# Optimization experiments

Measured on AMD Instinct MI355X. Metric: run time of the kernel, lower is better.

The kernel has to match this reference:

```python
import jax, jax.numpy as jnp
import numpy as np

B, S, D, H = 2, 2048, 1024, 16
DK = D // H


def setup_inputs() -> dict:
    key = jax.random.key(0)
    ks = jax.random.split(key, 6)
    scale = D ** -0.5
    return {
        "x": jax.random.normal(ks[0], (B, S, D), dtype=jnp.float32),
        "Wq": jax.random.normal(ks[1], (D, D), dtype=jnp.float32) * scale,
        "Wk": jax.random.normal(ks[2], (D, D), dtype=jnp.float32) * scale,
        "Wv": jax.random.normal(ks[3], (D, D), dtype=jnp.float32) * scale,
        "Wp": jax.random.normal(ks[4], (D, D), dtype=jnp.float32) * scale,
        "bp": jax.random.normal(ks[5], (D,), dtype=jnp.float32) * 0.01,
    }


def reference(x, Wq, Wk, Wv, Wp, bp):
    b, s, d = x.shape
    # projections (torch Linear: x @ W.T)
    q = (x @ Wq.T).reshape(b, s, H, DK).transpose(0, 2, 1, 3)  # [b,h,s,dk]
    k = (x @ Wk.T).reshape(b, s, H, DK).transpose(0, 2, 1, 3)
    v = (x @ Wv.T).reshape(b, s, H, DK).transpose(0, 2, 1, 3)
    wei = jnp.einsum('bhqd,bhkd->bhqk', q, k) * (DK ** -0.5)  # [b,h,s,s]
    causal = jnp.tril(jnp.ones((s, s), dtype=bool))
    wei = jnp.where(causal, wei, -jnp.inf)
    wei = jax.nn.softmax(wei, axis=-1)
    out = jnp.einsum('bhqk,bhkd->bhqd', wei, v)
    out = out.transpose(0, 2, 1, 3).reshape(b, s, H * DK)
    return out @ Wp.T + bp
```

## Files before the change

kernel.cpp:

```cpp
#include <hip/hip_runtime.h>
#include <hip/hip_bf16.h>

typedef short short8 __attribute__((ext_vector_type(8)));
typedef float floatx4 __attribute__((ext_vector_type(4)));
typedef float floatx16 __attribute__((ext_vector_type(16)));

#define DEV static __device__ __forceinline__

DEV unsigned short f2bf(float x) {
    union { float f; unsigned u; } v; v.f = x;
    unsigned r = v.u + 0x7FFFu + ((v.u >> 16) & 1u);
    return (unsigned short)(r >> 16);
}

DEV unsigned pk2(float lo, float hi) {
    union { __hip_bfloat162 h; unsigned u; } v;
    v.h = __float22bfloat162_rn(make_float2(lo, hi));
    return v.u;
}

DEV float fexp2(float x) {
#if __has_builtin(__builtin_amdgcn_exp2f)
    return __builtin_amdgcn_exp2f(x);
#else
    return exp2f(x);
#endif
}

DEV __attribute__((address_space(3))) unsigned int* lds_as3(void* p) {
    return (__attribute__((address_space(3))) unsigned int*)(unsigned int)(unsigned long long)p;
}
DEV const __attribute__((address_space(1))) unsigned int* gbl_as1(const void* p) {
    return (const __attribute__((address_space(1))) unsigned int*)(unsigned long long)p;
}

__global__ __launch_bounds__(256) void cvt_all(
    const float* __restrict__ x,  const float* __restrict__ wq,
    const float* __restrict__ wk, const float* __restrict__ wv,
    const float* __restrict__ wp,
    unsigned short* __restrict__ xb, unsigned short* __restrict__ wqkv,
    unsigned short* __restrict__ wpb)
{
    long c = (long)blockIdx.x * 256 + threadIdx.x;
    const float* src; unsigned short* dst; long off;
    if      (c <  524288) { src = x;  dst = xb;             off = c;          }
    else if (c <  655360) { src = wq; dst = wqkv;           off = c - 524288; }
    else if (c <  786432) { src = wk; dst = wqkv + 1048576; off = c - 655360; }
    else if (c <  917504) { src = wv; dst = wqkv + 2097152; off = c - 786432; }
    else                  { src = wp; dst = wpb;            off = c - 917504; }
    float4 a = ((const float4*)src)[off * 2];
    float4 b = ((const float4*)src)[off * 2 + 1];
    ushort4 r0, r1;
    r0.x = f2bf(a.x); r0.y = f2bf(a.y); r0.z = f2bf(a.z); r0.w = f2bf(a.w);
    r1.x = f2bf(b.x); r1.y = f2bf(b.y); r1.z = f2bf(b.z); r1.w = f2bf(b.w);
    ((ushort4*)dst)[off * 2]     = r0;
    ((ushort4*)dst)[off * 2 + 1] = r1;
}

template <int EPI>
__global__ __launch_bounds__(256) void gemm_bt(
    const unsigned short* __restrict__ A, const unsigned short* __restrict__ Bw,
    int M, int N, int K,
    unsigned short* __restrict__ Qd, unsigned short* __restrict__ Kd,
    unsigned short* __restrict__ Vtd,
    float* __restrict__ Cout, const float* __restrict__ bias)
{
    __shared__ unsigned short As[128 * 32];
    __shared__ unsigned short Bs[128 * 32];
    const int t    = threadIdx.x;
    const int lane = t & 63;
    const int wv   = t >> 6;
    const int wr   = (wv >> 1) * 64, wc = (wv & 1) * 64;
    const int lr   = lane & 15,      lg = lane >> 4;
    const int m0   = blockIdx.y * 128, n0 = blockIdx.x * 128;
    const int trow = t >> 2;
    const int tk   = (t & 3) * 8;

    floatx4 acc[4][4];
#pragma unroll
    for (int i = 0; i < 4; ++i)
#pragma unroll
        for (int j = 0; j < 4; ++j)
#pragma unroll
            for (int r = 0; r < 4; ++r) acc[i][j][r] = 0.f;

    for (int k0 = 0; k0 < K; k0 += 32) {
        __syncthreads();
#pragma unroll
        for (int r = 0; r < 2; ++r) {
            const unsigned short* ga = A  + (size_t)(m0 + r * 64 + trow) * K + k0 + tk;
            const unsigned short* gb = Bw + (size_t)(n0 + r * 64 + trow) * K + k0 + tk;
            __builtin_amdgcn_global_load_lds(gbl_as1(ga), lds_as3(&As[(r * 256 + t) * 8]), 16, 0, 0);
            __builtin_amdgcn_global_load_lds(gbl_as1(gb), lds_as3(&Bs[(r * 256 + t) * 8]), 16, 0, 0);
        }
        __syncthreads();
        short8 af[4], bf[4];
#pragma unroll
        for (int i = 0; i < 4; ++i) {
            af[i] = *(const short8*)&As[(wr + i * 16 + lr) * 32 + lg * 8];
            bf[i] = *(const short8*)&Bs[(wc + i * 16 + lr) * 32 + lg * 8];
        }
#pragma unroll
        for (int i = 0; i < 4; ++i)
#pragma unroll
            for (int j = 0; j < 4; ++j)
                acc[i][j] = __builtin_amdgcn_mfma_f32_16x16x32_bf16(af[i], bf[j], acc[i][j], 0, 0, 0);
    }

    if (EPI == 1) {
#pragma unroll
        for (int j = 0; j < 4; ++j) {
            int n = n0 + wc + j * 16 + lr;
            float bv = bias[n];
#pragma unroll
            for (int i = 0; i < 4; ++i) {
                int mb = m0 + wr + i * 16 + lg * 4;
#pragma unroll
                for (int r = 0; r < 4; ++r)
                    Cout[(size_t)(mb + r) * N + n] = acc[i][j][r] + bv;
            }
        }
    } else {
        const int which = n0 >> 10;
#pragma unroll
        for (int j = 0; j < 4; ++j) {
            int n = n0 + wc + j * 16 + lr;
            int h = (n & 1023) >> 6, d = n & 63;
#pragma unroll
            for (int i = 0; i < 4; ++i) {
                int mb = m0 + wr + i * 16 + lg * 4;
                int b = mb >> 11, s0 = mb & 2047;
                size_t bh = (size_t)(b * 16 + h);
                if (which == 2) {
                    ushort4 pv;
                    pv.x = f2bf(acc[i][j][0]); pv.y = f2bf(acc[i][j][1]);
                    pv.z = f2bf(acc[i][j][2]); pv.w = f2bf(acc[i][j][3]);
                    *(ushort4*)&Vtd[(bh * 64 + d) * 2048 + s0] = pv;
                } else {
                    unsigned short* dst = (which ? Kd : Qd) + (bh * 2048 + s0) * 64 + d;
#pragma unroll
                    for (int r = 0; r < 4; ++r) dst[r * 64] = f2bf(acc[i][j][r]);
                }
            }
        }
    }
}

__global__ __launch_bounds__(256) void attn_fwd(
    const unsigned short* __restrict__ Q, const unsigned short* __restrict__ Kg,
    const unsigned short* __restrict__ Vt, unsigned short* __restrict__ O)
{
    __shared__ unsigned short ot[4][32][80];
    const int bh = blockIdx.x;
    const int qt = 15 - blockIdx.y;
    const int t  = threadIdx.x, w = t >> 6, l = t & 63;
    const int lq = l & 31, hh = l >> 5;
    const int qw = qt * 128 + w * 32;
    const unsigned short* Qp = Q  + (size_t)bh * 2048 * 64;
    const unsigned short* Kp = Kg + (size_t)bh * 2048 * 64;
    const unsigned short* Vp = Vt + (size_t)bh * 64 * 2048;

    const float SCALE2 = 0.18033688011112042f;

    short8 qf[4];
#pragma unroll
    for (int kk = 0; kk < 4; ++kk)
        qf[kk] = *(const short8*)&Qp[(qw + lq) * 64 + kk * 16 + hh * 8];

    floatx16 o0, o1;
#pragma unroll
    for (int r = 0; r < 16; ++r) { o0[r] = 0.f; o1[r] = 0.f; }
    float mrun = -1e30f, lrun = 0.f;

    for (int kv0 = 0; kv0 <= qw; kv0 += 32) {
        floatx16 sa;
#pragma unroll
        for (int r = 0; r < 16; ++r) sa[r] = 0.f;
#pragma unroll
        for (int kk = 0; kk < 4; ++kk) {
            short8 kf = *(const short8*)&Kp[(kv0 + lq) * 64 + kk * 16 + hh * 8];
            sa = __builtin_amdgcn_mfma_f32_32x32x16_bf16(kf, qf[kk], sa, 0, 0, 0);
        }
        float sv[16];
        float tm = -1e30f;
        if (kv0 == qw) {
#pragma unroll
            for (int r = 0; r < 16; ++r) {
                int crow = (r & 3) + 8 * (r >> 2) + 4 * hh;
                float xx = sa[r] * SCALE2;
                if (crow > lq) xx = -1e30f;
                sv[r] = xx;
                tm = fmaxf(tm, xx);
            }
        } else {
#pragma unroll
            for (int r = 0; r < 16; ++r) {
                float xx = sa[r] * SCALE2;
                sv[r] = xx;
                tm = fmaxf(tm, xx);
            }
        }
        tm = fmaxf(tm, __shfl_xor(tm, 32));
        if (!__all(tm - mrun <= 8.f)) {
            float mn = fmaxf(mrun, tm);
            float f  = fexp2(mrun - mn);
            lrun *= f;
#pragma unroll
            for (int r = 0; r < 16; ++r) { o0[r] *= f; o1[r] *= f; }
            mrun = mn;
        }
        float ps = 0.f;
#pragma unroll
        for (int r = 0; r < 16; ++r) { sv[r] = fexp2(sv[r] - mrun); ps += sv[r]; }
        ps += __shfl_xor(ps, 32);
        lrun += ps;

#pragma unroll
        for (int c = 0; c < 2; ++c) {
            unsigned a0 = pk2(sv[c*8+0], sv[c*8+1]);
            unsigned a1 = pk2(sv[c*8+2], sv[c*8+3]);
            unsigned b0 = pk2(sv[c*8+4], sv[c*8+5]);
            unsigned b1 = pk2(sv[c*8+6], sv[c*8+7]);
            unsigned sa0 = __shfl_xor(a0, 32), sa1 = __shfl_xor(a1, 32);
            unsigned sb0 = __shfl_xor(b0, 32), sb1 = __shfl_xor(b1, 32);
            union { unsigned u[4]; short8 v; } pf;
            pf.u[0] = hh ? sb0 : a0;
            pf.u[1] = hh ? sb1 : a1;
            pf.u[2] = hh ? b0  : sa0;
            pf.u[3] = hh ? b1  : sa1;
            short8 vf0 = *(const short8*)&Vp[(size_t)(lq)      * 2048 + kv0 + c * 16 + hh * 8];
            short8 vf1 = *(const short8*)&Vp[(size_t)(32 + lq) * 2048 + kv0 + c * 16 + hh * 8];
            o0 = __builtin_amdgcn_mfma_f32_32x32x16_bf16(vf0, pf.v, o0, 0, 0, 0);
            o1 = __builtin_amdgcn_mfma_f32_32x32x16_bf16(vf1, pf.v, o1, 0, 0, 0);
        }
    }

    float inv = 1.f / lrun;
#pragma unroll
    for (int r = 0; r < 16; ++r) {
        int crow = (r & 3) + 8 * (r >> 2) + 4 * hh;
        ot[w][lq][crow]      = f2bf(o0[r] * inv);
        ot[w][lq][32 + crow] = f2bf(o1[r] * inv);
    }
    asm volatile("s_waitcnt lgkmcnt(0)" ::: "memory");
    const int b = bh >> 4, h = bh & 15;
    const int row = l >> 1, part = l & 1;
    size_t obase = (size_t)(b * 2048 + qt * 128 + w * 32 + row) * 1024 + h * 64 + part * 32;
#pragma unroll
    for (int jj = 0; jj < 4; ++jj) {
        uint4 v = *(const uint4*)&ot[w][row][part * 32 + jj * 8];
        *(uint4*)&O[obase + jj * 8] = v;
    }
}

extern "C" void kernel_launch(void* const* d_in, const int* in_sizes, int n_in,
                              void* d_out, int out_size, void* d_ws, size_t ws_size,
                              hipStream_t stream)
{
    const float* x  = (const float*)d_in[0];
    const float* Wq = (const float*)d_in[1];
    const float* Wk = (const float*)d_in[2];
    const float* Wv = (const float*)d_in[3];
    const float* Wp = (const float*)d_in[4];
    const float* bp = (const float*)d_in[5];
    float* out = (float*)d_out;

    char* ws = (char*)d_ws;
    unsigned short* xb   = (unsigned short*)(ws);
    unsigned short* wqkv = (unsigned short*)(ws + 8388608);
    unsigned short* wpb  = (unsigned short*)(ws + 14680064);
    unsigned short* Qw   = (unsigned short*)(ws + 16777216);
    unsigned short* Kw   = (unsigned short*)(ws + 25165824);
    unsigned short* Vtw  = (unsigned short*)(ws + 33554432);
    unsigned short* Ow   = (unsigned short*)(ws + 41943040);

    cvt_all<<<4096, 256, 0, stream>>>(x, Wq, Wk, Wv, Wp, xb, wqkv, wpb);
    gemm_bt<0><<<dim3(24, 32), 256, 0, stream>>>(xb, wqkv, 4096, 3072, 1024,
                                                 Qw, Kw, Vtw, nullptr, nullptr);
    attn_fwd<<<dim3(32, 16), 256, 0, stream>>>(Qw, Kw, Vtw, Ow);
    gemm_bt<1><<<dim3(8, 32), 256, 0, stream>>>(Ow, wpb, 4096, 1024, 1024,
                                                nullptr, nullptr, nullptr, out, bp);
}
```

Baseline: 234.9 us.

## Split causal attention KV range for late query tiles and merge partials

The attention kernel now runs in three z-slices. Early query tiles are computed fully. Late query tiles have their KV range split at 1024 into two partial passes, each writing unnormalized bf16 output plus running max and sum. A new merge kernel combines the two partials with log-sum-exp weights. This balances causal-triangle work across blocks to cut the tail imbalance, but adds an extra launch, partial-result traffic, and bf16 rounding of the unnormalized partials. It also reuses the xb and wqkv workspace regions as scratch.

```diff
diff --git a/kernel.cpp b/kernel.cpp
--- a/kernel.cpp
+++ b/kernel.cpp
@@ -25,6 +25,11 @@
 #else
     return exp2f(x);
 #endif
+}
+
+DEV float bf2f(unsigned short s) {
+    union { unsigned u; float f; } v; v.u = (unsigned)s << 16;
+    return v.f;
 }
 
 DEV __attribute__((address_space(3))) unsigned int* lds_as3(void* p) {
@@ -148,14 +153,18 @@
 
 __global__ __launch_bounds__(256) void attn_fwd(
     const unsigned short* __restrict__ Q, const unsigned short* __restrict__ Kg,
-    const unsigned short* __restrict__ Vt, unsigned short* __restrict__ O)
+    const unsigned short* __restrict__ Vt, unsigned short* __restrict__ O,
+    unsigned short* __restrict__ Opart, float* __restrict__ MLpart)
 {
     __shared__ unsigned short ot[4][32][80];
     const int bh = blockIdx.x;
-    const int qt = 15 - blockIdx.y;
+    const int z  = blockIdx.z;
+    const int qt = (z == 0) ? blockIdx.y : (8 + blockIdx.y);
     const int t  = threadIdx.x, w = t >> 6, l = t & 63;
     const int lq = l & 31, hh = l >> 5;
     const int qw = qt * 128 + w * 32;
+    const int kv0beg = (z == 2) ? 1024 : 0;
+    const int kvEnd  = (z == 1) ? 992  : qw;
     const unsigned short* Qp = Q  + (size_t)bh * 2048 * 64;
     const unsigned short* Kp = Kg + (size_t)bh * 2048 * 64;
     const unsigned short* Vp = Vt + (size_t)bh * 64 * 2048;
@@ -172,7 +181,7 @@
     for (int r = 0; r < 16; ++r) { o0[r] = 0.f; o1[r] = 0.f; }
     float mrun = -1e30f, lrun = 0.f;
 
-    for (int kv0 = 0; kv0 <= qw; kv0 += 32) {
+    for (int kv0 = kv0beg; kv0 <= kvEnd; kv0 += 32) {
         floatx16 sa;
 #pragma unroll
         for (int r = 0; r < 16; ++r) sa[r] = 0.f;
@@ -235,22 +244,72 @@
         }
     }
 
-    float inv = 1.f / lrun;
-#pragma unroll
-    for (int r = 0; r < 16; ++r) {
-        int crow = (r & 3) + 8 * (r >> 2) + 4 * hh;
-        ot[w][lq][crow]      = f2bf(o0[r] * inv);
-        ot[w][lq][32 + crow] = f2bf(o1[r] * inv);
+    if (z == 0) {
+        float inv = 1.f / lrun;
+#pragma unroll
+        for (int r = 0; r < 16; ++r) {
+            int crow = (r & 3) + 8 * (r >> 2) + 4 * hh;
+            ot[w][lq][crow]      = f2bf(o0[r] * inv);
+            ot[w][lq][32 + crow] = f2bf(o1[r] * inv);
+        }
+        asm volatile("s_waitcnt lgkmcnt(0)" ::: "memory");
+        const int b = bh >> 4, h = bh & 15;
+        const int row = l >> 1, part = l & 1;
+        size_t obase = (size_t)(b * 2048 + qw + row) * 1024 + h * 64 + part * 32;
+#pragma unroll
+        for (int jj = 0; jj < 4; ++jj) {
+            uint4 v = *(const uint4*)&ot[w][row][part * 32 + jj * 8];
+            *(uint4*)&O[obase + jj * 8] = v;
+        }
+    } else {
+        const size_t sb = (size_t)((z - 1) * 32 + bh) * 1024;
+        if (hh == 0)
+            *(float2*)&MLpart[(sb + (qw - 1024) + lq) * 2] = make_float2(mrun, lrun);
+#pragma unroll
+        for (int r = 0; r < 16; ++r) {
+            int crow = (r & 3) + 8 * (r >> 2) + 4 * hh;
+            ot[w][lq][crow]      = f2bf(o0[r]);
+            ot[w][lq][32 + crow] = f2bf(o1[r]);
+        }
+        asm volatile("s_waitcnt lgkmcnt(0)" ::: "memory");
+        const int row = l >> 1, part = l & 1;
+        size_t pbase = (sb + (qw - 1024) + row) * 64 + part * 32;
+#pragma unroll
+        for (int jj = 0; jj < 4; ++jj) {
+            uint4 v = *(const uint4*)&ot[w][row][part * 32 + jj * 8];
+            *(uint4*)&Opart[pbase + jj * 8] = v;
+        }
     }
-    asm volatile("s_waitcnt lgkmcnt(0)" ::: "memory");
-    const int b = bh >> 4, h = bh & 15;
-    const int row = l >> 1, part = l & 1;
-    size_t obase = (size_t)(b * 2048 + qt * 128 + w * 32 + row) * 1024 + h * 64 + part * 32;
-#pragma unroll
-    for (int jj = 0; jj < 4; ++jj) {
-        uint4 v = *(const uint4*)&ot[w][row][part * 32 + jj * 8];
-        *(uint4*)&O[obase + jj * 8] = v;
-    }
+}
+
+__global__ __launch_bounds__(256) void attn_merge(
+    const unsigned short* __restrict__ Opart, const float* __restrict__ MLpart,
+    unsigned short* __restrict__ O)
+{
+    const int tid = blockIdx.x * 256 + threadIdx.x;
+    const int c8  = (tid & 7) * 8;
+    const int q   = (tid >> 3) & 1023;
+    const int bh  = tid >> 13;
+    const size_t base = (size_t)bh * 1024 + q;
+
+    float2 ml0 = *(const float2*)&MLpart[base * 2];
+    float2 ml1 = *(const float2*)&MLpart[(32768 + base) * 2];
+    float M  = fmaxf(ml0.x, ml1.x);
+    float w0 = fexp2(ml0.x - M), w1 = fexp2(ml1.x - M);
+    float inv = 1.f / (w0 * ml0.y + w1 * ml1.y);
+    w0 *= inv; w1 *= inv;
+
+    short8 a = *(const short8*)&Opart[base * 64 + c8];
+    short8 b = *(const short8*)&Opart[(size_t)2097152 + base * 64 + c8];
+    float o[8];
+#pragma unroll
+    for (int j = 0; j < 8; ++j)
+        o[j] = w0 * bf2f((unsigned short)a[j]) + w1 * bf2f((unsigned short)b[j]);
+    uint4 ov;
+    ov.x = pk2(o[0], o[1]); ov.y = pk2(o[2], o[3]);
+    ov.z = pk2(o[4], o[5]); ov.w = pk2(o[6], o[7]);
+    const int bb = bh >> 4, h = bh & 15;
+    *(uint4*)&O[(size_t)(bb * 2048 + 1024 + q) * 1024 + h * 64 + c8] = ov;
 }
 
 extern "C" void kernel_launch(void* const* d_in, const int* in_sizes, int n_in,
@@ -273,11 +332,14 @@
     unsigned short* Kw   = (unsigned short*)(ws + 25165824);
     unsigned short* Vtw  = (unsigned short*)(ws + 33554432);
     unsigned short* Ow   = (unsigned short*)(ws + 41943040);
+    unsigned short* Opart = xb;
+    float*          MLp   = (float*)wqkv;
 
     cvt_all<<<4096, 256, 0, stream>>>(x, Wq, Wk, Wv, Wp, xb, wqkv, wpb);
     gemm_bt<0><<<dim3(24, 32), 256, 0, stream>>>(xb, wqkv, 4096, 3072, 1024,
                                                  Qw, Kw, Vtw, nullptr, nullptr);
-    attn_fwd<<<dim3(32, 16), 256, 0, stream>>>(Qw, Kw, Vtw, Ow);
+    attn_fwd<<<dim3(32, 8, 3), 256, 0, stream>>>(Qw, Kw, Vtw, Ow, Opart, MLp);
+    attn_merge<<<1024, 256, 0, stream>>>(Opart, MLp, Ow);
     gemm_bt<1><<<dim3(8, 32), 256, 0, stream>>>(Ow, wpb, 4096, 1024, 1024,
                                                 nullptr, nullptr, nullptr, out, bp);
 }
```

Result: no change. 237.0 us (+0.9%).
